# Kernel optimization log

Hardware: AMD Instinct MI355X
Metric: run time of the kernel (lower is better)

## Reference

```python
import jax, jax.numpy as jnp
import numpy as np

DIM = 1024
NUM_HEADS = 16
REL_DIM = 32
B, N = 8, 512


def setup_inputs() -> dict:
    key = jax.random.key(0)
    ks = jax.random.split(key, 8)
    s = 0.02
    return {
        "x": jax.random.normal(ks[0], (B, N, DIM), dtype=jnp.float32),
        "rel_bias": jax.random.normal(ks[1], (B, N, N, REL_DIM), dtype=jnp.float32),
        # torch nn.Linear convention: weight (out_features, in_features)
        "W_qkv": jax.random.normal(ks[2], (3 * DIM, DIM), dtype=jnp.float32) * s,
        "b_qkv": jax.random.normal(ks[3], (3 * DIM,), dtype=jnp.float32) * s,
        "W_rel": jax.random.normal(ks[4], (NUM_HEADS, REL_DIM), dtype=jnp.float32) * s,
        "b_rel": jax.random.normal(ks[5], (NUM_HEADS,), dtype=jnp.float32) * s,
        "W_out": jax.random.normal(ks[6], (DIM, DIM), dtype=jnp.float32) * s,
        "b_out": jax.random.normal(ks[7], (DIM,), dtype=jnp.float32) * s,
    }


def reference(x, rel_bias, W_qkv, b_qkv, W_rel, b_rel, W_out, b_out):
    Bx, Nx, D = x.shape
    H = NUM_HEADS
    hd = D // H
    # QKV projection: (B,N,3D) -> (B,N,3,H,hd)
    qkv = (x @ W_qkv.T + b_qkv).reshape(Bx, Nx, 3, H, hd)
    q, k, v = qkv[:, :, 0], qkv[:, :, 1], qkv[:, :, 2]
    scale = hd ** -0.5
    attn = jnp.einsum('bnhd,bmhd->bhnm', q, k) * scale
    # per-pair relative bias projected to heads: (B,N,N,H) -> (B,H,N,N)
    rel = (rel_bias @ W_rel.T + b_rel).transpose(0, 3, 1, 2)
    attn = jax.nn.softmax(attn + rel, axis=-1)
    out = jnp.einsum('bhnm,bmhd->bnhd', attn, v).reshape(Bx, Nx, D)
    return out @ W_out.T + b_out
```

## Files before the change

kernel.cpp:

```cpp
#include <hip/hip_runtime.h>

typedef unsigned short u16;
typedef unsigned int u32;
typedef __attribute__((ext_vector_type(8))) __bf16 bf16x8;
typedef __attribute__((ext_vector_type(4))) float f32x4;

union U8 {
  bf16x8 b;
  uint2 u2[2];
  uint4 u4;
  u32 w[4];
  u16 us[8];
};

__device__ __forceinline__ u16 f2bf(float f) {
  u32 x = __float_as_uint(f);
  x += 0x7FFFu + ((x >> 16) & 1u);
  return (u16)(x >> 16);
}
__device__ __forceinline__ float bf2f(u16 u) {
  return __uint_as_float(((u32)u) << 16);
}
__device__ __forceinline__ u32 cvtpk(float lo, float hi) {
  u32 r;
  asm("v_cvt_pk_bf16_f32 %0, %1, %2" : "=v"(r) : "v"(lo), "v"(hi));
  return r;
}

#define GLOAD16(gp, lp)                                                          \
  __builtin_amdgcn_global_load_lds(                                              \
      (const __attribute__((address_space(1))) unsigned int*)(const void*)(gp),  \
      (__attribute__((address_space(3))) unsigned int*)(void*)(lp), 16, 0, 0)

__global__ void k_convert_all(const float* __restrict__ x, const float* __restrict__ wq,
                              const float* __restrict__ wo, u16* __restrict__ xb,
                              u16* __restrict__ wqb, u16* __restrict__ wob) {
  const int NX = 1048576, NQ = 786432, NO = 262144;
  int idx = blockIdx.x * blockDim.x + threadIdx.x;
  int stride = gridDim.x * blockDim.x;
  for (int i = idx; i < NX + NQ + NO; i += stride) {
    const float4* s;
    ushort4* d;
    int k;
    if (i < NX) { s = (const float4*)x; d = (ushort4*)xb; k = i; }
    else if (i < NX + NQ) { s = (const float4*)wq; d = (ushort4*)wqb; k = i - NX; }
    else { s = (const float4*)wo; d = (ushort4*)wob; k = i - NX - NQ; }
    float4 v = s[k];
    ushort4 o;
    o.x = f2bf(v.x); o.y = f2bf(v.y); o.z = f2bf(v.z); o.w = f2bf(v.w);
    d[k] = o;
  }
}

__global__ __launch_bounds__(256) void k_rel(const float* __restrict__ rb,
                                             const float* __restrict__ Wr,
                                             const float* __restrict__ br,
                                             u16* __restrict__ out) {
  const int t = threadIdx.x;
  const int lane = t & 63, c2 = t >> 6;
  const int i16 = lane & 15, g4 = lane >> 4;
  const int mt = blockIdx.x, nt = blockIdx.y, b = blockIdx.z;

  U8 wb;
  {
    const float* wp = Wr + i16 * 32 + 8 * g4;
    float4 w0 = *(const float4*)wp;
    float4 w1 = *(const float4*)(wp + 4);
    wb.w[0] = cvtpk(w0.x, w0.y);
    wb.w[1] = cvtpk(w0.z, w0.w);
    wb.w[2] = cvtpk(w1.x, w1.y);
    wb.w[3] = cvtpk(w1.z, w1.w);
  }
  const float bias = br[i16];

  const int m = mt * 64 + c2 * 16 + i16;
  const float* rbase = rb + ((size_t)(b * 512 + nt * 16) * 512 + m) * 32 + 8 * g4;

  f32x4 accv[16];
#pragma unroll
  for (int ni = 0; ni < 16; ++ni) {
    float4 a0 = *(const float4*)(rbase + (size_t)ni * 16384);
    float4 a1 = *(const float4*)(rbase + (size_t)ni * 16384 + 4);
    U8 af;
    af.w[0] = cvtpk(a0.x, a0.y);
    af.w[1] = cvtpk(a0.z, a0.w);
    af.w[2] = cvtpk(a1.x, a1.y);
    af.w[3] = cvtpk(a1.z, a1.w);
    f32x4 ci = {bias, bias, bias, bias};
    accv[ni] = __builtin_amdgcn_mfma_f32_16x16x32_bf16(af.b, wb.b, ci, 0, 0, 0);
  }

  const size_t base =
      ((((size_t)(b * 16 + i16)) * 32 + nt) * 8 + mt) * 1024 + c2 * 256 + g4 * 16;
#pragma unroll
  for (int gp = 0; gp < 4; ++gp) {
    u32 wd[8];
#pragma unroll
    for (int w = 0; w < 8; ++w) {
      int jj = w >> 1, jlo = 2 * (w & 1);
      wd[w] = cvtpk(accv[4 * gp + jlo][jj], accv[4 * gp + jlo + 1][jj]);
    }
    uint4 s0 = {wd[0], wd[1], wd[2], wd[3]};
    uint4 s1 = {wd[4], wd[5], wd[6], wd[7]};
    *(uint4*)(out + base + gp * 64) = s0;
    *(uint4*)(out + base + gp * 64 + 8) = s1;
  }
}

__global__ __launch_bounds__(256) void k_gemm_qkv(const u16* __restrict__ A,
                                                  const u16* __restrict__ Bm,
                                                  const float* __restrict__ bias,
                                                  u16* __restrict__ Qo, u16* __restrict__ Ko,
                                                  u16* __restrict__ Vo) {
  const int K = 1024;
  __shared__ u16 Al[128 * 64];
  __shared__ u16 Bl[128 * 64];
  const int t = threadIdx.x;
  const int lane = t & 63, wid = t >> 6;
  const int g = lane >> 4, i16 = lane & 15;
  const int wm = wid >> 1, wn = wid & 1;
  const int bm = blockIdx.y, bn = blockIdx.x;

  f32x4 zero = {0.f, 0.f, 0.f, 0.f};
  f32x4 acc[4][4];
#pragma unroll
  for (int mi = 0; mi < 4; ++mi)
#pragma unroll
    for (int ni = 0; ni < 4; ++ni) acc[mi][ni] = zero;

  int srow[4], sgc[4];
#pragma unroll
  for (int i = 0; i < 4; ++i) {
    int ch = wid * 256 + i * 64 + lane;
    int r = ch >> 3, cs = ch & 7;
    srow[i] = r;
    sgc[i] = cs ^ (r & 7);
  }

  for (int k0 = 0; k0 < K; k0 += 64) {
    __syncthreads();
#pragma unroll
    for (int i = 0; i < 4; ++i) {
      const u16* ga = A + (size_t)(bm * 128 + srow[i]) * K + k0 + sgc[i] * 8;
      const u16* gb = Bm + (size_t)(bn * 128 + srow[i]) * K + k0 + sgc[i] * 8;
      GLOAD16(ga, Al + (size_t)(wid * 256 + i * 64) * 8);
      GLOAD16(gb, Bl + (size_t)(wid * 256 + i * 64) * 8);
    }
    __syncthreads();

#pragma unroll
    for (int kk = 0; kk < 2; ++kk) {
      U8 af[4], bfr[4];
#pragma unroll
      for (int mi = 0; mi < 4; ++mi) {
        int row = wm * 64 + mi * 16 + i16;
        int ch = (g + 4 * kk) ^ (row & 7);
        af[mi].u4 = *(const uint4*)(Al + row * 64 + ch * 8);
      }
#pragma unroll
      for (int ni = 0; ni < 4; ++ni) {
        int row = wn * 64 + ni * 16 + i16;
        int ch = (g + 4 * kk) ^ (row & 7);
        bfr[ni].u4 = *(const uint4*)(Bl + row * 64 + ch * 8);
      }
#pragma unroll
      for (int mi = 0; mi < 4; ++mi)
#pragma unroll
        for (int ni = 0; ni < 4; ++ni)
          acc[mi][ni] = __builtin_amdgcn_mfma_f32_16x16x32_bf16(af[mi].b, bfr[ni].b,
                                                                acc[mi][ni], 0, 0, 0);
    }
  }

#pragma unroll
  for (int mi = 0; mi < 4; ++mi) {
#pragma unroll
    for (int ni = 0; ni < 4; ++ni) {
      int col = bn * 128 + wn * 64 + ni * 16 + i16;
      int row0 = bm * 128 + wm * 64 + mi * 16 + 4 * g;
      float bia = bias[col];
      int tt = col >> 10;
      int h = (col >> 6) & 15;
      int d = col & 63;
      int b = row0 >> 9;
      int n0 = row0 & 511;
      if (tt < 2) {
        u16* dst = (tt == 0) ? Qo : Ko;
#pragma unroll
        for (int j = 0; j < 4; ++j)
          dst[((size_t)(b * 16 + h) * 512 + n0 + j) * 64 + d] = f2bf(acc[mi][ni][j] + bia);
      } else {
        uint2 w;
        w.x = cvtpk(acc[mi][ni][0] + bia, acc[mi][ni][1] + bia);
        w.y = cvtpk(acc[mi][ni][2] + bia, acc[mi][ni][3] + bia);
        *(uint2*)(Vo + ((size_t)(b * 16 + h) * 64 + d) * 512 + n0) = w;
      }
    }
  }
}

__global__ __launch_bounds__(256) void k_gemm_out(const u16* __restrict__ A,
                                                  const u16* __restrict__ Bm,
                                                  const float* __restrict__ bias,
                                                  float* __restrict__ Co) {
  const int K = 1024;
  __shared__ u16 Al[128 * 64];
  __shared__ u16 Bl[64 * 64];
  const int t = threadIdx.x;
  const int lane = t & 63, wid = t >> 6;
  const int g = lane >> 4, i16 = lane & 15;
  const int bm = blockIdx.y, bn = blockIdx.x;

  f32x4 zero = {0.f, 0.f, 0.f, 0.f};
  f32x4 acc[2][4];
#pragma unroll
  for (int mi = 0; mi < 2; ++mi)
#pragma unroll
    for (int ni = 0; ni < 4; ++ni) acc[mi][ni] = zero;

  int srowA[4], sgcA[4], srowB[2], sgcB[2];
#pragma unroll
  for (int i = 0; i < 4; ++i) {
    int ch = wid * 256 + i * 64 + lane;
    int r = ch >> 3, cs = ch & 7;
    srowA[i] = r;
    sgcA[i] = cs ^ (r & 7);
  }
#pragma unroll
  for (int i = 0; i < 2; ++i) {
    int ch = wid * 128 + i * 64 + lane;
    int r = ch >> 3, cs = ch & 7;
    srowB[i] = r;
    sgcB[i] = cs ^ (r & 7);
  }

  for (int k0 = 0; k0 < K; k0 += 64) {
    __syncthreads();
#pragma unroll
    for (int i = 0; i < 4; ++i)
      GLOAD16(A + (size_t)(bm * 128 + srowA[i]) * K + k0 + sgcA[i] * 8,
              Al + (size_t)(wid * 256 + i * 64) * 8);
#pragma unroll
    for (int i = 0; i < 2; ++i)
      GLOAD16(Bm + (size_t)(bn * 64 + srowB[i]) * K + k0 + sgcB[i] * 8,
              Bl + (size_t)(wid * 128 + i * 64) * 8);
    __syncthreads();

#pragma unroll
    for (int kk = 0; kk < 2; ++kk) {
      U8 af[2], bfr[4];
#pragma unroll
      for (int mi = 0; mi < 2; ++mi) {
        int row = wid * 32 + mi * 16 + i16;
        int ch = (g + 4 * kk) ^ (row & 7);
        af[mi].u4 = *(const uint4*)(Al + row * 64 + ch * 8);
      }
#pragma unroll
      for (int ni = 0; ni < 4; ++ni) {
        int row = ni * 16 + i16;
        int ch = (g + 4 * kk) ^ (row & 7);
        bfr[ni].u4 = *(const uint4*)(Bl + row * 64 + ch * 8);
      }
#pragma unroll
      for (int mi = 0; mi < 2; ++mi)
#pragma unroll
        for (int ni = 0; ni < 4; ++ni)
          acc[mi][ni] = __builtin_amdgcn_mfma_f32_16x16x32_bf16(af[mi].b, bfr[ni].b,
                                                                acc[mi][ni], 0, 0, 0);
    }
  }

#pragma unroll
  for (int mi = 0; mi < 2; ++mi) {
#pragma unroll
    for (int ni = 0; ni < 4; ++ni) {
      int col = bn * 64 + ni * 16 + i16;
      int row0 = bm * 128 + wid * 32 + mi * 16 + 4 * g;
      float bia = bias[col];
#pragma unroll
      for (int j = 0; j < 4; ++j)
        Co[(size_t)(row0 + j) * 1024 + col] = acc[mi][ni][j] + bia;
    }
  }
}

__global__ __launch_bounds__(256) void k_attn(const u16* __restrict__ Q,
                                              const u16* __restrict__ Kb,
                                              const u16* __restrict__ Vtb,
                                              const u16* __restrict__ Rel,
                                              u16* __restrict__ Out) {
  __shared__ u16 Kl[2][64 * 64];
  __shared__ u16 Vl[2][64 * 64];
  __shared__ u16 Pl[4][16 * 68];

  const int qt = blockIdx.x, h = blockIdx.y, b = blockIdx.z;
  const int t = threadIdx.x, lane = t & 63, wid = t >> 6;
  const int g = lane >> 4, i16 = lane & 15;
  const size_t bh = (size_t)(b * 16 + h);

  const u16* Qg = Q + (bh * 512 + qt * 64 + wid * 16 + i16) * 64;
  U8 qf[2];
  qf[0].u4 = *(const uint4*)(Qg + 8 * g);
  qf[1].u4 = *(const uint4*)(Qg + 8 * g + 32);

  float m_run[4], l_run[4];
  f32x4 zero = {0.f, 0.f, 0.f, 0.f};
  f32x4 acc[4];
#pragma unroll
  for (int c = 0; c < 4; ++c) acc[c] = zero;
#pragma unroll
  for (int j = 0; j < 4; ++j) { m_run[j] = -1e30f; l_run[j] = 0.f; }

  int srow[2], sgc[2];
#pragma unroll
  for (int i = 0; i < 2; ++i) {
    int ch = wid * 128 + i * 64 + lane;
    int r = ch >> 3, cs = ch & 7;
    srow[i] = r;
    sgc[i] = cs ^ (r & 7);
  }

  const u16* Kg0 = Kb + bh * 512 * 64;
  const u16* Vg0 = Vtb + bh * 64 * 512;
  const u16* Rg = Rel + ((bh * 32 + qt * 4 + wid) * 8) * 1024 + lane * 4;

#define STAGE(buf, m0)                                                                  \
  do {                                                                                  \
    _Pragma("unroll") for (int i = 0; i < 2; ++i) {                                     \
      GLOAD16(Kg0 + (size_t)((m0) + srow[i]) * 64 + sgc[i] * 8,                         \
              &Kl[buf][(size_t)(wid * 128 + i * 64) * 8]);                              \
      GLOAD16(Vg0 + (size_t)srow[i] * 512 + (m0) + sgc[i] * 8,                          \
              &Vl[buf][(size_t)(wid * 128 + i * 64) * 8]);                              \
    }                                                                                   \
  } while (0)

  STAGE(0, 0);
  __syncthreads();

  for (int it = 0; it < 8; ++it) {
    const int buf = it & 1;
    if (it < 7) STAGE(buf ^ 1, it * 64 + 64);

    uint2 rl[4];
#pragma unroll
    for (int c = 0; c < 4; ++c) rl[c] = *(const uint2*)(Rg + it * 1024 + c * 256);

    f32x4 s[4];
#pragma unroll
    for (int c = 0; c < 4; ++c) s[c] = zero;
    __builtin_amdgcn_s_setprio(1);
#pragma unroll
    for (int c = 0; c < 4; ++c) {
#pragma unroll
      for (int kk = 0; kk < 2; ++kk) {
        int row = c * 16 + i16;
        int ch = (g + 4 * kk) ^ (row & 7);
        U8 kf;
        kf.u4 = *(const uint4*)(&Kl[buf][row * 64 + ch * 8]);
        s[c] = __builtin_amdgcn_mfma_f32_16x16x32_bf16(qf[kk].b, kf.b, s[c], 0, 0, 0);
      }
    }
    __builtin_amdgcn_s_setprio(0);

#pragma unroll
    for (int c = 0; c < 4; ++c) {
      const u16* rc = (const u16*)&rl[c];
#pragma unroll
      for (int j = 0; j < 4; ++j) s[c][j] = s[c][j] * 0.125f + bf2f(rc[j]);
    }
    float fac[4];
#pragma unroll
    for (int j = 0; j < 4; ++j) {
      float pm = fmaxf(fmaxf(s[0][j], s[1][j]), fmaxf(s[2][j], s[3][j]));
      pm = fmaxf(pm, __shfl_xor(pm, 1));
      pm = fmaxf(pm, __shfl_xor(pm, 2));
      pm = fmaxf(pm, __shfl_xor(pm, 4));
      pm = fmaxf(pm, __shfl_xor(pm, 8));
      float mnew = fmaxf(m_run[j], pm);
      fac[j] = __expf(m_run[j] - mnew);
      m_run[j] = mnew;
    }
#pragma unroll
    for (int c = 0; c < 4; ++c)
#pragma unroll
      for (int j = 0; j < 4; ++j) s[c][j] = __expf(s[c][j] - m_run[j]);
#pragma unroll
    for (int j = 0; j < 4; ++j) {
      float rs = s[0][j] + s[1][j] + s[2][j] + s[3][j];
      rs += __shfl_xor(rs, 1);
      rs += __shfl_xor(rs, 2);
      rs += __shfl_xor(rs, 4);
      rs += __shfl_xor(rs, 8);
      l_run[j] = l_run[j] * fac[j] + rs;
    }
#pragma unroll
    for (int c = 0; c < 4; ++c)
#pragma unroll
      for (int j = 0; j < 4; ++j) acc[c][j] *= fac[j];

    u16* Pw = Pl[wid];
#pragma unroll
    for (int c = 0; c < 4; ++c)
#pragma unroll
      for (int j = 0; j < 4; ++j)
        Pw[(4 * g + j) * 68 + c * 16 + i16] = f2bf(s[c][j]);
    __syncthreads();

    U8 pf[2];
#pragma unroll
    for (int kk = 0; kk < 2; ++kk) {
      const u16* p = Pl[wid] + i16 * 68 + 8 * g + 32 * kk;
      pf[kk].u2[0] = *(const uint2*)p;
      pf[kk].u2[1] = *(const uint2*)(p + 4);
    }
    __builtin_amdgcn_s_setprio(1);
#pragma unroll
    for (int c = 0; c < 4; ++c) {
#pragma unroll
      for (int kk = 0; kk < 2; ++kk) {
        int row = c * 16 + i16;
        int ch = (g + 4 * kk) ^ (row & 7);
        U8 vf;
        vf.u4 = *(const uint4*)(&Vl[buf][row * 64 + ch * 8]);
        acc[c] = __builtin_amdgcn_mfma_f32_16x16x32_bf16(pf[kk].b, vf.b, acc[c], 0, 0, 0);
      }
    }
    __builtin_amdgcn_s_setprio(0);
    __syncthreads();
  }
#undef STAGE

#pragma unroll
  for (int c = 0; c < 4; ++c) {
#pragma unroll
    for (int j = 0; j < 4; ++j) {
      int n = qt * 64 + wid * 16 + 4 * g + j;
      float v = acc[c][j] / l_run[j];
      Out[((size_t)b * 512 + n) * 1024 + h * 64 + c * 16 + i16] = f2bf(v);
    }
  }
}

extern "C" void kernel_launch(void* const* d_in, const int* in_sizes, int n_in,
                              void* d_out, int out_size, void* d_ws, size_t ws_size,
                              hipStream_t stream) {
  const float* x = (const float*)d_in[0];
  const float* rel_bias = (const float*)d_in[1];
  const float* W_qkv = (const float*)d_in[2];
  const float* b_qkv = (const float*)d_in[3];
  const float* W_rel = (const float*)d_in[4];
  const float* b_rel = (const float*)d_in[5];
  const float* W_out = (const float*)d_in[6];
  const float* b_out = (const float*)d_in[7];
  float* out = (float*)d_out;

  char* ws = (char*)d_ws;
  u16* x_bf    = (u16*)(ws);
  u16* wqkv_bf = (u16*)(ws + 8388608);
  u16* wout_bf = (u16*)(ws + 14680064);
  u16* Qw      = (u16*)(ws + 16777216);
  u16* Kw      = (u16*)(ws + 25165824);
  u16* Vt      = (u16*)(ws + 33554432);
  u16* relb    = (u16*)(ws + 41943040);
  u16* attno   = (u16*)(ws + 109051904);

  k_convert_all<<<2048, 256, 0, stream>>>(x, W_qkv, W_out, x_bf, wqkv_bf, wout_bf);

  k_rel<<<dim3(8, 32, 8), 256, 0, stream>>>(rel_bias, W_rel, b_rel, relb);

  k_gemm_qkv<<<dim3(24, 32), 256, 0, stream>>>(x_bf, wqkv_bf, b_qkv, Qw, Kw, Vt);

  k_attn<<<dim3(8, 16, 8), 256, 0, stream>>>(Qw, Kw, Vt, relb, attno);

  k_gemm_out<<<dim3(16, 32), 256, 0, stream>>>(attno, wout_bf, b_out, out);
}
```

Measured before the change: 200.0 us.

## Enlarge output GEMM tile to 128x128 and interleave rel-bias loads with stores

The output projection GEMM now uses 128x128 block tiles with a 2x2 warp layout, and each warp computes 64x64. This doubles operand reuse per LDS load and halves the grid to 256 blocks. The rel-bias kernel now loads, converts and stores in groups of four instead of holding all 16 accumulators before storing, which lowers register pressure. The cost is fewer blocks on a GPU with many CUs, which may leave CUs idle, plus more accumulator registers in the GEMM.

Result: no change. 202.4 us (+1.2%).

```diff
diff --git a/kernel.cpp b/kernel.cpp
--- a/kernel.cpp
+++ b/kernel.cpp
@@ -75,30 +75,30 @@
 
   const int m = mt * 64 + c2 * 16 + i16;
   const float* rbase = rb + ((size_t)(b * 512 + nt * 16) * 512 + m) * 32 + 8 * g4;
-
-  f32x4 accv[16];
-#pragma unroll
-  for (int ni = 0; ni < 16; ++ni) {
-    float4 a0 = *(const float4*)(rbase + (size_t)ni * 16384);
-    float4 a1 = *(const float4*)(rbase + (size_t)ni * 16384 + 4);
-    U8 af;
-    af.w[0] = cvtpk(a0.x, a0.y);
-    af.w[1] = cvtpk(a0.z, a0.w);
-    af.w[2] = cvtpk(a1.x, a1.y);
-    af.w[3] = cvtpk(a1.z, a1.w);
-    f32x4 ci = {bias, bias, bias, bias};
-    accv[ni] = __builtin_amdgcn_mfma_f32_16x16x32_bf16(af.b, wb.b, ci, 0, 0, 0);
-  }
-
   const size_t base =
       ((((size_t)(b * 16 + i16)) * 32 + nt) * 8 + mt) * 1024 + c2 * 256 + g4 * 16;
+
 #pragma unroll
   for (int gp = 0; gp < 4; ++gp) {
+    f32x4 accv[4];
+#pragma unroll
+    for (int k = 0; k < 4; ++k) {
+      int ni = 4 * gp + k;
+      float4 a0 = *(const float4*)(rbase + (size_t)ni * 16384);
+      float4 a1 = *(const float4*)(rbase + (size_t)ni * 16384 + 4);
+      U8 af;
+      af.w[0] = cvtpk(a0.x, a0.y);
+      af.w[1] = cvtpk(a0.z, a0.w);
+      af.w[2] = cvtpk(a1.x, a1.y);
+      af.w[3] = cvtpk(a1.z, a1.w);
+      f32x4 ci = {bias, bias, bias, bias};
+      accv[k] = __builtin_amdgcn_mfma_f32_16x16x32_bf16(af.b, wb.b, ci, 0, 0, 0);
+    }
     u32 wd[8];
 #pragma unroll
     for (int w = 0; w < 8; ++w) {
       int jj = w >> 1, jlo = 2 * (w & 1);
-      wd[w] = cvtpk(accv[4 * gp + jlo][jj], accv[4 * gp + jlo + 1][jj]);
+      wd[w] = cvtpk(accv[jlo][jj], accv[jlo + 1][jj]);
     }
     uint4 s0 = {wd[0], wd[1], wd[2], wd[3]};
     uint4 s1 = {wd[4], wd[5], wd[6], wd[7]};
@@ -205,64 +205,57 @@
                                                   float* __restrict__ Co) {
   const int K = 1024;
   __shared__ u16 Al[128 * 64];
-  __shared__ u16 Bl[64 * 64];
+  __shared__ u16 Bl[128 * 64];
   const int t = threadIdx.x;
   const int lane = t & 63, wid = t >> 6;
   const int g = lane >> 4, i16 = lane & 15;
+  const int wm = wid >> 1, wn = wid & 1;
   const int bm = blockIdx.y, bn = blockIdx.x;
 
   f32x4 zero = {0.f, 0.f, 0.f, 0.f};
-  f32x4 acc[2][4];
-#pragma unroll
-  for (int mi = 0; mi < 2; ++mi)
+  f32x4 acc[4][4];
+#pragma unroll
+  for (int mi = 0; mi < 4; ++mi)
 #pragma unroll
     for (int ni = 0; ni < 4; ++ni) acc[mi][ni] = zero;
 
-  int srowA[4], sgcA[4], srowB[2], sgcB[2];
+  int srow[4], sgc[4];
 #pragma unroll
   for (int i = 0; i < 4; ++i) {
     int ch = wid * 256 + i * 64 + lane;
     int r = ch >> 3, cs = ch & 7;
-    srowA[i] = r;
-    sgcA[i] = cs ^ (r & 7);
-  }
-#pragma unroll
-  for (int i = 0; i < 2; ++i) {
-    int ch = wid * 128 + i * 64 + lane;
-    int r = ch >> 3, cs = ch & 7;
-    srowB[i] = r;
-    sgcB[i] = cs ^ (r & 7);
+    srow[i] = r;
+    sgc[i] = cs ^ (r & 7);
   }
 
   for (int k0 = 0; k0 < K; k0 += 64) {
     __syncthreads();
 #pragma unroll
-    for (int i = 0; i < 4; ++i)
-      GLOAD16(A + (size_t)(bm * 128 + srowA[i]) * K + k0 + sgcA[i] * 8,
+    for (int i = 0; i < 4; ++i) {
+      GLOAD16(A + (size_t)(bm * 128 + srow[i]) * K + k0 + sgc[i] * 8,
               Al + (size_t)(wid * 256 + i * 64) * 8);
-#pragma unroll
-    for (int i = 0; i < 2; ++i)
-      GLOAD16(Bm + (size_t)(bn * 64 + srowB[i]) * K + k0 + sgcB[i] * 8,
-              Bl + (size_t)(wid * 128 + i * 64) * 8);
+      GLOAD16(Bm + (size_t)(bn * 128 + srow[i]) * K + k0 + sgc[i] * 8,
+              Bl + (size_t)(wid * 256 + i * 64) * 8);
+    }
     __syncthreads();
 
 #pragma unroll
     for (int kk = 0; kk < 2; ++kk) {
-      U8 af[2], bfr[4];
-#pragma unroll
-      for (int mi = 0; mi < 2; ++mi) {
-        int row = wid * 32 + mi * 16 + i16;
+      U8 af[4], bfr[4];
+#pragma unroll
+      for (int mi = 0; mi < 4; ++mi) {
+        int row = wm * 64 + mi * 16 + i16;
         int ch = (g + 4 * kk) ^ (row & 7);
         af[mi].u4 = *(const uint4*)(Al + row * 64 + ch * 8);
       }
 #pragma unroll
       for (int ni = 0; ni < 4; ++ni) {
-        int row = ni * 16 + i16;
+        int row = wn * 64 + ni * 16 + i16;
         int ch = (g + 4 * kk) ^ (row & 7);
         bfr[ni].u4 = *(const uint4*)(Bl + row * 64 + ch * 8);
       }
 #pragma unroll
-      for (int mi = 0; mi < 2; ++mi)
+      for (int mi = 0; mi < 4; ++mi)
 #pragma unroll
         for (int ni = 0; ni < 4; ++ni)
           acc[mi][ni] = __builtin_amdgcn_mfma_f32_16x16x32_bf16(af[mi].b, bfr[ni].b,
@@ -271,11 +264,11 @@
   }
 
 #pragma unroll
-  for (int mi = 0; mi < 2; ++mi) {
+  for (int mi = 0; mi < 4; ++mi) {
 #pragma unroll
     for (int ni = 0; ni < 4; ++ni) {
-      int col = bn * 64 + ni * 16 + i16;
-      int row0 = bm * 128 + wid * 32 + mi * 16 + 4 * g;
+      int col = bn * 128 + wn * 64 + ni * 16 + i16;
+      int row0 = bm * 128 + wm * 64 + mi * 16 + 4 * g;
       float bia = bias[col];
 #pragma unroll
       for (int j = 0; j < 4; ++j)
@@ -472,5 +465,5 @@
 
   k_attn<<<dim3(8, 16, 8), 256, 0, stream>>>(Qw, Kw, Vt, relb, attno);
 
-  k_gemm_out<<<dim3(16, 32), 256, 0, stream>>>(attno, wout_bf, b_out, out);
-}
+  k_gemm_out<<<dim3(8, 32), 256, 0, stream>>>(attno, wout_bf, b_out, out);
+}
```
